# Performance work log

Hardware: AMD Instinct MI355X
Metric: run time of the kernel (lower is better)

Reference implementation:

```python
import jax, jax.numpy as jnp
import numpy as np

N = 50000      # nodes
E = 500000     # edges
H = 128        # hidden_channels
P = 1024       # number of (src,dst) link pairs: z==1 and z==2 counts
L = 3          # num_layers
MAXZ = 1000


def setup_inputs() -> dict:
    key = jax.random.key(0)
    ks = jax.random.split(key, 16)
    # z: P src nodes (label 1), P dst nodes (label 2), rest random labels >= 3
    z = jnp.concatenate([
        jnp.ones((P,), jnp.int32),
        jnp.full((P,), 2, jnp.int32),
        jax.random.randint(ks[0], (N - 2 * P,), 3, MAXZ, dtype=jnp.int32),
    ])
    edge_index = jax.random.randint(ks[1], (2, E), 0, N, dtype=jnp.int32)
    batch = jnp.zeros((N,), jnp.int32)  # unused in executed branch
    s = 1.0 / np.sqrt(H)
    z_table = jax.random.normal(ks[2], (MAXZ, H), jnp.float32) * 0.1
    conv_Wl = jax.random.normal(ks[3], (L, H, H), jnp.float32) * s
    conv_bl = jax.random.normal(ks[4], (L, H), jnp.float32) * 0.01
    conv_Wr = jax.random.normal(ks[5], (L, H, H), jnp.float32) * s
    W0 = jax.random.normal(ks[6], (H, H), jnp.float32) * s
    b0 = jax.random.normal(ks[7], (H,), jnp.float32) * 0.01
    W1 = jax.random.normal(ks[8], (H, H), jnp.float32) * s
    b1 = jax.random.normal(ks[9], (H,), jnp.float32) * 0.01
    W2 = jax.random.normal(ks[10], (1, H), jnp.float32) * s
    b2 = jax.random.normal(ks[11], (1,), jnp.float32) * 0.01
    return dict(z=z, edge_index=edge_index, batch=batch, z_table=z_table,
                conv_Wl=conv_Wl, conv_bl=conv_bl, conv_Wr=conv_Wr,
                W0=W0, b0=b0, W1=W1, b1=b1, W2=W2, b2=b2)


def _sage_conv(x, Wl, bl, Wr, src, dst):
    # x: [2, N, H]; mean-aggregate neighbor messages then linear (PyG SAGEConv)
    msgs = x[:, src, :]  # [2, E, H] gather
    agg = jax.vmap(lambda m: jax.ops.segment_sum(m, dst, num_segments=N))(msgs)
    deg = jax.ops.segment_sum(jnp.ones((dst.shape[0],), x.dtype), dst, num_segments=N)
    agg = agg / jnp.maximum(deg, 1.0)[None, :, None]
    return agg @ Wl.T + bl + x @ Wr.T  # lin_l(mean) + bias + lin_r(x)


def reference(z, edge_index, batch, z_table, conv_Wl, conv_bl, conv_Wr,
              W0, b0, W1, b1, W2, b2):
    src, dst = edge_index[0], edge_index[1]
    # ([[1],[2]] == z).long() -> [2, N] in {0,1}; embed -> [2, N, H]
    lbl = (jnp.arange(1, 3, dtype=z.dtype)[:, None] == z[None, :]).astype(jnp.int32)
    x = z_table[lbl]
    for i in range(L - 1):
        x = jax.nn.relu(_sage_conv(x, conv_Wl[i], conv_bl[i], conv_Wr[i], src, dst))
    x = _sage_conv(x, conv_Wl[L - 1], conv_bl[L - 1], conv_Wr[L - 1], src, dst)
    h = jax.nn.relu(x @ W0.T + b0).sum(axis=0)  # [N, H]
    src_idx = jnp.nonzero(z == 1, size=P)[0]
    dst_idx = jnp.nonzero(z == 2, size=P)[0]
    p = h[src_idx] * h[dst_idx]                 # [P, H]
    return jax.nn.relu(p @ W1.T + b1) @ W2.T + b2  # [P, 1]
```

## Files before the change

### kernel.cpp

```cpp
#include <hip/hip_runtime.h>
#include <stdint.h>

#define HH 128
typedef unsigned long long ull;
typedef unsigned short u16;

__device__ __forceinline__ ull shfl_up64(ull v, int d) {
  unsigned lo = (unsigned)__shfl_up((int)(unsigned)(v & 0xffffffffULL), d);
  unsigned hi = (unsigned)__shfl_up((int)(unsigned)(v >> 32), d);
  return ((ull)hi << 32) | (ull)lo;
}
__device__ __forceinline__ ull shfl_down64(ull v, int d) {
  unsigned lo = (unsigned)__shfl_down((int)(unsigned)(v & 0xffffffffULL), d);
  unsigned hi = (unsigned)__shfl_down((int)(unsigned)(v >> 32), d);
  return ((ull)hi << 32) | (ull)lo;
}

__global__ __launch_bounds__(256) void k_ytab(
    const float* __restrict__ zt, const float* __restrict__ Wl0,
    const float* __restrict__ Wr0, const float* __restrict__ Wl2,
    const float* __restrict__ Wr2, const float* __restrict__ bl0,
    const float* __restrict__ bl1, float* __restrict__ y_l,
    float* __restrict__ y_rb, float* __restrict__ vecs_g,
    const int* __restrict__ z, int N, ull* __restrict__ cnt64,
    int* __restrict__ mark) {
  __shared__ float ztS[2][HH];
  __shared__ float vS[4][HH];
  __shared__ float xS[16][HH];
  int t = threadIdx.x;
  {
    int gid = blockIdx.x * 256 + t;
    int nthr = gridDim.x * 256;
    for (int n = gid; n < N; n += nthr) {
      cnt64[n] = 0ULL;
      mark[n] = (z[n] <= 2) ? 1 : 0;
    }
  }
  ztS[t >> 7][t & 127] = zt[t];
  __syncthreads();
#pragma unroll
  for (int rep = 0; rep < 2; rep++) {
    int idx = t + rep * 256;
    int m = idx >> 7, j = idx & 127;
    const float* W = (m < 2) ? Wl0 : Wr0;
    const float* zrow = ztS[m & 1];
    float acc = 0.f;
    for (int k = 0; k < HH; k++) acc = fmaf(zrow[k], W[j * HH + k], acc);
    vS[m][j] = acc;
  }
  __syncthreads();
  if (blockIdx.x == 0) {
    vecs_g[t] = vS[t >> 7][t & 127];
    vecs_g[256 + t] = vS[2 + (t >> 7)][t & 127];
  }
  int v0 = blockIdx.x * 16;
#pragma unroll
  for (int rep = 0; rep < 8; rep++) {
    int idx = t + rep * 256;
    int r = idx >> 7, j = idx & 127;
    int v = v0 + r;
    int d = v >> 4, cnt = (v >> 1) & 7, sel = v & 1;
    float invd = 1.0f / (float)max(d, 1);
    float u1 = (float)cnt * invd, u0 = (float)(d - cnt) * invd;
    xS[r][j] = fmaxf(fmaf(u0, vS[0][j], fmaf(u1, vS[1][j], bl0[j] + vS[2 + sel][j])), 0.f);
  }
  __syncthreads();
  int j = t & 127, rh = t >> 7;
  float al[8], ar[8];
#pragma unroll
  for (int q = 0; q < 8; q++) { al[q] = 0.f; ar[q] = 0.f; }
  for (int k = 0; k < HH; k++) {
    float wl = Wl2[j * HH + k], wr = Wr2[j * HH + k];
#pragma unroll
    for (int q = 0; q < 8; q++) {
      float x = xS[rh * 8 + q][k];
      al[q] = fmaf(x, wl, al[q]);
      ar[q] = fmaf(x, wr, ar[q]);
    }
  }
  float bb = bl1[j];
#pragma unroll
  for (int q = 0; q < 8; q++) {
    int v = v0 + rh * 8 + q;
    y_l[((size_t)v << 7) + j] = al[q];
    y_rb[((size_t)v << 7) + j] = ar[q] + bb;
  }
}

__global__ void k_edge(const int* __restrict__ z, const int* __restrict__ src,
                       const int* __restrict__ dst, int E,
                       ull* __restrict__ cnt64, int* __restrict__ mark,
                       int* __restrict__ pos) {
  int tid = blockIdx.x * blockDim.x + threadIdx.x;
  int stride = gridDim.x * blockDim.x;
  for (int e = tid; e < E; e += stride) {
    int s = src[e], d = dst[e];
    int zs = z[s];
    ull val = 1ULL | ((ull)(zs == 1) << 20) | ((ull)(zs == 2) << 40);
    ull old = atomicAdd(&cnt64[d], val);
    pos[e] = (int)(old & 0xFFFFF);
    if (z[d] <= 2) mark[s] = 1;
  }
}

__global__ void k_scan1(const ull* __restrict__ cnt64, const int* __restrict__ mark,
                        const int* __restrict__ z, int N,
                        ull* __restrict__ locout, ull* __restrict__ partials) {
  __shared__ ull wsum[4];
  int t = threadIdx.x, b = blockIdx.x;
  int base = b * 1024 + t * 4;
  ull l[4]; ull s = 0;
  for (int i = 0; i < 4; i++) {
    int idx = base + i; ull v = 0;
    if (idx < N) {
      int zz = z[idx];
      v = (cnt64[idx] & 0xFFFFFULL) | ((ull)mark[idx] << 20)
        | ((ull)(zz == 1) << 40) | ((ull)(zz == 2) << 52);
    }
    l[i] = s; s += v;
  }
  int lane = t & 63, wid = t >> 6;
  ull vi = s;
  for (int d2 = 1; d2 < 64; d2 <<= 1) { ull o = shfl_up64(vi, d2); if (lane >= d2) vi += o; }
  if (lane == 63) wsum[wid] = vi;
  __syncthreads();
  ull woff = 0;
  for (int w = 0; w < wid; w++) woff += wsum[w];
  ull thrbase = woff + vi - s;
  for (int i = 0; i < 4; i++) {
    int idx = base + i;
    if (idx < N) locout[idx] = thrbase + l[i];
  }
  if (t == 255) partials[b] = woff + vi;
}

__global__ __launch_bounds__(256) void k_post(const ull* __restrict__ locout, const ull* __restrict__ partials,
                       const int* __restrict__ z, const int* __restrict__ mark,
                       const ull* __restrict__ cnt64,
                       int N, int P, int* __restrict__ rowptr, int* __restrict__ mlist,
                       int* __restrict__ minv, int* __restrict__ plist,
                       int* __restrict__ Rm, int4* __restrict__ pack,
                       u16* __restrict__ keyN) {
  __shared__ ull base_s;
  int t = threadIdx.x;
  if (t < 64) {
    int need = blockIdx.x >> 2;
    ull v = (t < need) ? partials[t] : 0ULL;
    for (int o = 32; o > 0; o >>= 1) v += shfl_down64(v, o);
    if (t == 0) base_s = v;
  }
  __syncthreads();
  int n = blockIdx.x * 256 + t;
  if (n >= N) return;
  ull s = locout[n] + base_s;
  int rp = (int)(s & 0xFFFFF);
  int mp = (int)((s >> 20) & 0xFFFFF);
  int r1 = (int)((s >> 40) & 0xFFF);
  int r2 = (int)(s >> 52);
  rowptr[n] = rp;
  int mk = mark[n];
  if (mk) { mlist[mp] = n; minv[n] = mp; }
  int zz = z[n];
  if (zz == 1) plist[r1] = n;
  else if (zz == 2) plist[P + r2] = n;
  ull cv = cnt64[n];
  int dd = (int)(cv & 0xFFFFF), c1 = (int)((cv >> 20) & 0xFFFFF), c2 = (int)((cv >> 40) & 0xFFFFF);
  pack[n] = make_int4(dd, c1, c2, zz);
  int wcls = (zz == 1) ? 1 : ((zz == 2) ? 2 : 0);
  u16 key;
  if (dd < 64 && c1 < 8 && c2 < 8) key = (u16)(dd | (c1 << 6) | (c2 << 9) | (wcls << 12));
  else key = 0x8000;
  keyN[n] = key;
  if (n == N - 1) *Rm = mp + mk;
}

__global__ void k_csrk(const int* __restrict__ src, const int* __restrict__ dst, int E,
                       const int* __restrict__ rowptr, const int* __restrict__ pos,
                       const u16* __restrict__ keyN, ull* __restrict__ csrk) {
  int e = blockIdx.x * blockDim.x + threadIdx.x;
  if (e >= E) return;
  int d = dst[e], s = src[e];
  csrk[rowptr[d] + pos[e]] = (ull)(unsigned)s | ((ull)keyN[s] << 32);
}

__device__ __noinline__ float4 yrow_fb(const float* __restrict__ vecs,
    const float* __restrict__ bl0, const float* __restrict__ Wm,
    int j4, int d, int cnt, int sel) {
  float invd = 1.0f / (float)max(d, 1);
  float u1 = (float)cnt * invd, u0 = (float)(d - cnt) * invd;
  const float* Rv = vecs + (2 + sel) * HH;
  float4 acc = make_float4(0, 0, 0, 0);
  for (int k = 0; k < HH; k++) {
    float x = fmaxf(fmaf(u0, vecs[k], fmaf(u1, vecs[HH + k], bl0[k] + Rv[k])), 0.f);
    acc.x = fmaf(x, Wm[(j4 + 0) * HH + k], acc.x);
    acc.y = fmaf(x, Wm[(j4 + 1) * HH + k], acc.y);
    acc.z = fmaf(x, Wm[(j4 + 2) * HH + k], acc.z);
    acc.w = fmaf(x, Wm[(j4 + 3) * HH + k], acc.w);
  }
  return acc;
}

__device__ __forceinline__ float4 yl_fetch(ull cv, int ch, int chsel, int j4,
    const float* __restrict__ y_l, const int4* __restrict__ pack,
    const float* __restrict__ vecs, const float* __restrict__ bl0,
    const float* __restrict__ Wl2) {
  int key = (int)(cv >> 32);
  if (key & 0x8000) {
    int s = (int)(cv & 0xFFFFFFFFULL);
    int4 p = pack[s];
    int cc = ch ? p.z : p.y;
    int sel = (p.w == chsel) ? 1 : 0;
    return yrow_fb(vecs, bl0, Wl2, j4, p.x, cc, sel);
  }
  int cc = (key >> (6 + 3 * ch)) & 7;
  int sel = (((key >> 12) & 3) == chsel) ? 1 : 0;
  int row = ((key & 63) << 4) + (cc << 1) + sel;
  return *(const float4*)(y_l + ((size_t)row << 7) + j4);
}

__global__ __launch_bounds__(256) void k_agg2Y(const int4* __restrict__ pack,
    const ull* __restrict__ csrk, const float* __restrict__ y_l,
    const float* __restrict__ y_rb, const float* __restrict__ vecs,
    const float* __restrict__ bl0, const float* __restrict__ bl1,
    const float* __restrict__ Wl2, const float* __restrict__ Wr2,
    const int* __restrict__ rowptr, const int* __restrict__ mlist,
    const int* __restrict__ Rdev, float* __restrict__ x2c) {
  int gt = blockIdx.x * blockDim.x + threadIdx.x;
  int w = gt >> 6, lane = gt & 63;
  int nw = (gridDim.x * blockDim.x) >> 6;
  int T = *Rdev;
  int ch = lane >> 5, j4 = (lane & 31) * 4;
  int chsel = ch + 1;
  for (int task = w; task < T; task += nw) {
    int n = mlist[task];
    int4 pn = pack[n];
    int beg = rowptr[n], d = pn.x;
    float4 acc = make_float4(0, 0, 0, 0);
    int i = 0;
    for (; i + 4 <= d; i += 4) {
      ull c0 = csrk[beg + i], c1 = csrk[beg + i + 1];
      ull c2 = csrk[beg + i + 2], c3 = csrk[beg + i + 3];
      float4 v0 = yl_fetch(c0, ch, chsel, j4, y_l, pack, vecs, bl0, Wl2);
      float4 v1 = yl_fetch(c1, ch, chsel, j4, y_l, pack, vecs, bl0, Wl2);
      float4 v2 = yl_fetch(c2, ch, chsel, j4, y_l, pack, vecs, bl0, Wl2);
      float4 v3 = yl_fetch(c3, ch, chsel, j4, y_l, pack, vecs, bl0, Wl2);
      acc.x += v0.x + v1.x + v2.x + v3.x;
      acc.y += v0.y + v1.y + v2.y + v3.y;
      acc.z += v0.z + v1.z + v2.z + v3.z;
      acc.w += v0.w + v1.w + v2.w + v3.w;
    }
    for (; i < d; i++) {
      float4 v0 = yl_fetch(csrk[beg + i], ch, chsel, j4, y_l, pack, vecs, bl0, Wl2);
      acc.x += v0.x; acc.y += v0.y; acc.z += v0.z; acc.w += v0.w;
    }
    float inv = 1.0f / (float)max(d, 1);
    int ccn = ch ? pn.z : pn.y;
    int seln = (pn.w == chsel) ? 1 : 0;
    float4 yr;
    if (pn.x < 64 && ccn < 8) {
      yr = *(const float4*)(y_rb + ((size_t)(((pn.x << 3) + ccn) * 2 + seln) << 7) + j4);
    } else {
      yr = yrow_fb(vecs, bl0, Wr2, j4, pn.x, ccn, seln);
      yr.x += bl1[j4]; yr.y += bl1[j4 + 1]; yr.z += bl1[j4 + 2]; yr.w += bl1[j4 + 3];
    }
    float4 o;
    o.x = fmaxf(fmaf(acc.x, inv, yr.x), 0.f);
    o.y = fmaxf(fmaf(acc.y, inv, yr.y), 0.f);
    o.z = fmaxf(fmaf(acc.z, inv, yr.z), 0.f);
    o.w = fmaxf(fmaf(acc.w, inv, yr.w), 0.f);
    *(float4*)(x2c + (size_t)task * 256 + ch * HH + j4) = o;
  }
}

__global__ __launch_bounds__(256) void k_agg3(const float* __restrict__ x2c,
    const ull* __restrict__ csrk, const int* __restrict__ rowptr,
    const int4* __restrict__ pack, const int* __restrict__ plist,
    const int* __restrict__ minv, int T, float* __restrict__ aggp) {
  int gt = blockIdx.x * blockDim.x + threadIdx.x;
  int w = gt >> 6, lane = gt & 63;
  int nw = (gridDim.x * blockDim.x) >> 6;
  int j4 = lane * 4;
  for (int task = w; task < T; task += nw) {
    int n = plist[task];
    int beg = rowptr[n], d = pack[n].x;
    float4 acc = make_float4(0, 0, 0, 0);
    int i = 0;
    for (; i + 4 <= d; i += 4) {
      int m0 = minv[(int)(csrk[beg + i] & 0xFFFFFFFFULL)];
      int m1 = minv[(int)(csrk[beg + i + 1] & 0xFFFFFFFFULL)];
      int m2 = minv[(int)(csrk[beg + i + 2] & 0xFFFFFFFFULL)];
      int m3 = minv[(int)(csrk[beg + i + 3] & 0xFFFFFFFFULL)];
      float4 v0 = *(const float4*)(x2c + (size_t)m0 * 256 + j4);
      float4 v1 = *(const float4*)(x2c + (size_t)m1 * 256 + j4);
      float4 v2 = *(const float4*)(x2c + (size_t)m2 * 256 + j4);
      float4 v3 = *(const float4*)(x2c + (size_t)m3 * 256 + j4);
      acc.x += v0.x + v1.x + v2.x + v3.x;
      acc.y += v0.y + v1.y + v2.y + v3.y;
      acc.z += v0.z + v1.z + v2.z + v3.z;
      acc.w += v0.w + v1.w + v2.w + v3.w;
    }
    for (; i < d; i++) {
      int m0 = minv[(int)(csrk[beg + i] & 0xFFFFFFFFULL)];
      float4 v0 = *(const float4*)(x2c + (size_t)m0 * 256 + j4);
      acc.x += v0.x; acc.y += v0.y; acc.z += v0.z; acc.w += v0.w;
    }
    float inv = 1.0f / (float)max(d, 1);
    float4 o = make_float4(acc.x * inv, acc.y * inv, acc.z * inv, acc.w * inv);
    *(float4*)(aggp + (size_t)task * 256 + j4) = o;
  }
}

#define G3 4
__global__ __launch_bounds__(256) void k_gemm3F(const float* __restrict__ aggp,
    const float* __restrict__ x2c, const float* __restrict__ Wl3,
    const float* __restrict__ Wr3, const float* __restrict__ W0,
    const float* __restrict__ bl2, const float* __restrict__ b0,
    const int* __restrict__ plist, const int* __restrict__ minv,
    float* __restrict__ tmp0) {
  __shared__ float aS[G3][256], xS[G3][256], x3S[G3][256];
  __shared__ float wAS[32][HH + 1], wBS[32][HH + 1];
  int t = threadIdx.x;
  int i0 = blockIdx.x * G3;
  int j = t & 127, c = t >> 7;
#pragma unroll
  for (int g = 0; g < G3; g++) {
    int i = i0 + g;
    aS[g][t] = aggp[(size_t)i * 256 + t];
    xS[g][t] = x2c[(size_t)minv[plist[i]] * 256 + t];
  }
  float acc[G3];
#pragma unroll
  for (int g = 0; g < G3; g++) acc[g] = bl2[j];
  int jw = t >> 3;
  int kk0 = (t & 7) * 4;
  for (int kt = 0; kt < 4; kt++) {
    __syncthreads();
#pragma unroll
    for (int q = 0; q < 4; q++) {
      int jj = q * 32 + jw;
      float4 va = *(const float4*)(Wl3 + (size_t)jj * HH + kt * 32 + kk0);
      float4 vb = *(const float4*)(Wr3 + (size_t)jj * HH + kt * 32 + kk0);
      wAS[kk0 + 0][jj] = va.x; wAS[kk0 + 1][jj] = va.y;
      wAS[kk0 + 2][jj] = va.z; wAS[kk0 + 3][jj] = va.w;
      wBS[kk0 + 0][jj] = vb.x; wBS[kk0 + 1][jj] = vb.y;
      wBS[kk0 + 2][jj] = vb.z; wBS[kk0 + 3][jj] = vb.w;
    }
    __syncthreads();
#pragma unroll
    for (int kk = 0; kk < 32; kk++) {
      int k = kt * 32 + kk;
      float wl = wAS[kk][j], wr = wBS[kk][j];
#pragma unroll
      for (int g = 0; g < G3; g++)
        acc[g] = fmaf(aS[g][c * HH + k], wl, fmaf(xS[g][c * HH + k], wr, acc[g]));
    }
  }
#pragma unroll
  for (int g = 0; g < G3; g++) x3S[g][t] = acc[g];
  float acc2[G3];
#pragma unroll
  for (int g = 0; g < G3; g++) acc2[g] = b0[j];
  for (int kt = 0; kt < 4; kt++) {
    __syncthreads();
#pragma unroll
    for (int q = 0; q < 4; q++) {
      int jj = q * 32 + jw;
      float4 v0 = *(const float4*)(W0 + (size_t)jj * HH + kt * 32 + kk0);
      wAS[kk0 + 0][jj] = v0.x; wAS[kk0 + 1][jj] = v0.y;
      wAS[kk0 + 2][jj] = v0.z; wAS[kk0 + 3][jj] = v0.w;
    }
    __syncthreads();
#pragma unroll
    for (int kk = 0; kk < 32; kk++) {
      int k = kt * 32 + kk;
      float w0v = wAS[kk][j];
#pragma unroll
      for (int g = 0; g < G3; g++)
        acc2[g] = fmaf(x3S[g][c * HH + k], w0v, acc2[g]);
    }
  }
#pragma unroll
  for (int g = 0; g < G3; g++)
    tmp0[(size_t)(2 * (i0 + g) + c) * HH + j] = fmaxf(acc2[g], 0.f);
}

__global__ __launch_bounds__(256) void k_finalP(const float* __restrict__ tmp0,
    const float* __restrict__ W1, const float* __restrict__ b1,
    const float* __restrict__ W2, const float* __restrict__ b2,
    int P, float* __restrict__ out) {
  __shared__ float pS[2][HH];
  __shared__ float wred[4];
  int t = threadIdx.x;
  int half = t >> 7, j = t & 127;
  int i = blockIdx.x * 2 + half;
  float hs = tmp0[(size_t)(2 * i) * HH + j] + tmp0[(size_t)(2 * i + 1) * HH + j];
  float hd = tmp0[(size_t)(2 * (i + P)) * HH + j] + tmp0[(size_t)(2 * (i + P) + 1) * HH + j];
  pS[half][j] = hs * hd;
  __syncthreads();
  float acc = b1[j];
#pragma unroll 8
  for (int k = 0; k < HH; k++) acc = fmaf(pS[half][k], W1[j * HH + k], acc);
  float v = fmaxf(acc, 0.f) * W2[j];
  for (int off = 32; off > 0; off >>= 1) v += __shfl_down(v, off);
  int wid = t >> 6, lane = t & 63;
  if (lane == 0) wred[wid] = v;
  __syncthreads();
  if (t == 0) out[i] = wred[0] + wred[1] + b2[0];
  else if (t == 128) out[i] = wred[2] + wred[3] + b2[0];
}

extern "C" void kernel_launch(void* const* d_in, const int* in_sizes, int n_in,
                              void* d_out, int out_size, void* d_ws, size_t ws_size,
                              hipStream_t stream) {
  const int* z = (const int*)d_in[0];
  const int* ei = (const int*)d_in[1];
  const float* z_table = (const float*)d_in[3];
  const float* conv_Wl = (const float*)d_in[4];
  const float* conv_bl = (const float*)d_in[5];
  const float* conv_Wr = (const float*)d_in[6];
  const float* W0 = (const float*)d_in[7];
  const float* b0 = (const float*)d_in[8];
  const float* W1 = (const float*)d_in[9];
  const float* b1 = (const float*)d_in[10];
  const float* W2 = (const float*)d_in[11];
  const float* b2 = (const float*)d_in[12];
  float* out = (float*)d_out;

  int N = in_sizes[0];
  int E = in_sizes[1] / 2;
  int P = out_size;
  int P2 = 2 * P;
  const int* srcA = ei;
  const int* dstA = ei + E;

  char* basep = (char*)d_ws;
  size_t off = 0;
  auto alloc = [&](size_t bytes) -> char* {
    off = (off + 255) & ~(size_t)255;
    char* pp = basep + off; off += bytes; return pp;
  };
  float* y_l   = (float*)alloc((size_t)1024 * HH * 4);
  float* y_rb  = (float*)alloc((size_t)1024 * HH * 4);
  float* vecs  = (float*)alloc((size_t)4 * HH * 4);
  float* x2c   = (float*)alloc((size_t)N * 256 * 4);
  float* aggp  = (float*)alloc((size_t)P2 * 256 * 4);
  float* tmp0  = (float*)alloc((size_t)2 * P2 * HH * 4);
  ull*   cnt64 = (ull*)alloc((size_t)N * 8);
  int*   mark  = (int*)alloc((size_t)N * 4);
  int*   pos   = (int*)alloc((size_t)E * 4);
  int*   rowptr= (int*)alloc((size_t)N * 4);
  int*   mlist = (int*)alloc((size_t)N * 4);
  int*   minv  = (int*)alloc((size_t)N * 4);
  int*   plist = (int*)alloc((size_t)P2 * 4);
  ull*   csrk  = (ull*)alloc((size_t)E * 8);
  ull*   locout= (ull*)alloc((size_t)N * 8);
  ull*   partials = (ull*)alloc(256 * 8);
  int*   Rm_dev = (int*)alloc(256);
  u16*   keyN  = (u16*)alloc((size_t)N * 2);
  int4*  pack  = (int4*)alloc((size_t)N * 16);
  (void)ws_size; (void)n_in;

  k_ytab<<<64, 256, 0, stream>>>(z_table, conv_Wl, conv_Wr,
                                 conv_Wl + HH * HH, conv_Wr + HH * HH,
                                 conv_bl, conv_bl + HH, y_l, y_rb, vecs,
                                 z, N, cnt64, mark);
  k_edge<<<1024, 256, 0, stream>>>(z, srcA, dstA, E, cnt64, mark, pos);
  int nb = (N + 1023) / 1024;
  k_scan1<<<nb, 256, 0, stream>>>(cnt64, mark, z, N, locout, partials);
  k_post<<<(N + 255) / 256, 256, 0, stream>>>(locout, partials, z, mark, cnt64, N, P,
                                              rowptr, mlist, minv, plist, Rm_dev, pack, keyN);
  k_csrk<<<(E + 255) / 256, 256, 0, stream>>>(srcA, dstA, E, rowptr, pos, keyN, csrk);
  k_agg2Y<<<2048, 256, 0, stream>>>(pack, csrk, y_l, y_rb, vecs, conv_bl, conv_bl + HH,
                                    conv_Wl + HH * HH, conv_Wr + HH * HH,
                                    rowptr, mlist, Rm_dev, x2c);
  k_agg3<<<512, 256, 0, stream>>>(x2c, csrk, rowptr, pack, plist, minv, P2, aggp);
  k_gemm3F<<<P2 / G3, 256, 0, stream>>>(aggp, x2c, conv_Wl + 2 * HH * HH,
                                        conv_Wr + 2 * HH * HH, W0,
                                        conv_bl + 2 * HH, b0, plist, minv, tmp0);
  k_finalP<<<P / 2, 256, 0, stream>>>(tmp0, W1, b1, W2, b2, P, out);
}
```

Baseline: 132.7 us.

## Stage weight tiles in LDS with coalesced loads; skip CSR writes for unmarked dsts

```diff
diff --git a/kernel.cpp b/kernel.cpp
--- a/kernel.cpp
+++ b/kernel.cpp
@@ -27,6 +27,7 @@
   __shared__ float ztS[2][HH];
   __shared__ float vS[4][HH];
   __shared__ float xS[16][HH];
+  __shared__ float wAS[32][HH + 1], wBS[32][HH + 1];
   int t = threadIdx.x;
   {
     int gid = blockIdx.x * 256 + t;
@@ -38,16 +39,32 @@
   }
   ztS[t >> 7][t & 127] = zt[t];
   __syncthreads();
-#pragma unroll
-  for (int rep = 0; rep < 2; rep++) {
-    int idx = t + rep * 256;
-    int m = idx >> 7, j = idx & 127;
-    const float* W = (m < 2) ? Wl0 : Wr0;
-    const float* zrow = ztS[m & 1];
-    float acc = 0.f;
-    for (int k = 0; k < HH; k++) acc = fmaf(zrow[k], W[j * HH + k], acc);
-    vS[m][j] = acc;
-  }
+  int j = t & 127, half = t >> 7;
+  int jw = t >> 3, kk0 = (t & 7) * 4;
+  float accA = 0.f, accR = 0.f;
+  for (int kt = 0; kt < 4; kt++) {
+    __syncthreads();
+#pragma unroll
+    for (int q = 0; q < 4; q++) {
+      int jj = q * 32 + jw;
+      float4 va = *(const float4*)(Wl0 + (size_t)jj * HH + kt * 32 + kk0);
+      float4 vb = *(const float4*)(Wr0 + (size_t)jj * HH + kt * 32 + kk0);
+      wAS[kk0 + 0][jj] = va.x; wAS[kk0 + 1][jj] = va.y;
+      wAS[kk0 + 2][jj] = va.z; wAS[kk0 + 3][jj] = va.w;
+      wBS[kk0 + 0][jj] = vb.x; wBS[kk0 + 1][jj] = vb.y;
+      wBS[kk0 + 2][jj] = vb.z; wBS[kk0 + 3][jj] = vb.w;
+    }
+    __syncthreads();
+#pragma unroll
+    for (int kk = 0; kk < 32; kk++) {
+      float zk = ztS[half][kt * 32 + kk];
+      accA = fmaf(zk, wAS[kk][j], accA);
+      accR = fmaf(zk, wBS[kk][j], accR);
+    }
+  }
+  __syncthreads();
+  vS[half][j] = accA;
+  vS[2 + half][j] = accR;
   __syncthreads();
   if (blockIdx.x == 0) {
     vecs_g[t] = vS[t >> 7][t & 127];
@@ -57,25 +74,39 @@
 #pragma unroll
   for (int rep = 0; rep < 8; rep++) {
     int idx = t + rep * 256;
-    int r = idx >> 7, j = idx & 127;
+    int r = idx >> 7, jx = idx & 127;
     int v = v0 + r;
     int d = v >> 4, cnt = (v >> 1) & 7, sel = v & 1;
     float invd = 1.0f / (float)max(d, 1);
     float u1 = (float)cnt * invd, u0 = (float)(d - cnt) * invd;
-    xS[r][j] = fmaxf(fmaf(u0, vS[0][j], fmaf(u1, vS[1][j], bl0[j] + vS[2 + sel][j])), 0.f);
-  }
-  __syncthreads();
-  int j = t & 127, rh = t >> 7;
+    xS[r][jx] = fmaxf(fmaf(u0, vS[0][jx], fmaf(u1, vS[1][jx], bl0[jx] + vS[2 + sel][jx])), 0.f);
+  }
+  int rh = t >> 7;
   float al[8], ar[8];
 #pragma unroll
   for (int q = 0; q < 8; q++) { al[q] = 0.f; ar[q] = 0.f; }
-  for (int k = 0; k < HH; k++) {
-    float wl = Wl2[j * HH + k], wr = Wr2[j * HH + k];
-#pragma unroll
-    for (int q = 0; q < 8; q++) {
-      float x = xS[rh * 8 + q][k];
-      al[q] = fmaf(x, wl, al[q]);
-      ar[q] = fmaf(x, wr, ar[q]);
+  for (int kt = 0; kt < 4; kt++) {
+    __syncthreads();
+#pragma unroll
+    for (int q = 0; q < 4; q++) {
+      int jj = q * 32 + jw;
+      float4 va = *(const float4*)(Wl2 + (size_t)jj * HH + kt * 32 + kk0);
+      float4 vb = *(const float4*)(Wr2 + (size_t)jj * HH + kt * 32 + kk0);
+      wAS[kk0 + 0][jj] = va.x; wAS[kk0 + 1][jj] = va.y;
+      wAS[kk0 + 2][jj] = va.z; wAS[kk0 + 3][jj] = va.w;
+      wBS[kk0 + 0][jj] = vb.x; wBS[kk0 + 1][jj] = vb.y;
+      wBS[kk0 + 2][jj] = vb.z; wBS[kk0 + 3][jj] = vb.w;
+    }
+    __syncthreads();
+#pragma unroll
+    for (int kk = 0; kk < 32; kk++) {
+      float wl = wAS[kk][j], wr = wBS[kk][j];
+#pragma unroll
+      for (int q = 0; q < 8; q++) {
+        float x = xS[rh * 8 + q][kt * 32 + kk];
+        al[q] = fmaf(x, wl, al[q]);
+        ar[q] = fmaf(x, wr, ar[q]);
+      }
     }
   }
   float bb = bl1[j];
@@ -176,10 +207,13 @@
 
 __global__ void k_csrk(const int* __restrict__ src, const int* __restrict__ dst, int E,
                        const int* __restrict__ rowptr, const int* __restrict__ pos,
-                       const u16* __restrict__ keyN, ull* __restrict__ csrk) {
+                       const u16* __restrict__ keyN, const int* __restrict__ mark,
+                       ull* __restrict__ csrk) {
   int e = blockIdx.x * blockDim.x + threadIdx.x;
   if (e >= E) return;
-  int d = dst[e], s = src[e];
+  int d = dst[e];
+  if (!mark[d]) return;
+  int s = src[e];
   csrk[rowptr[d] + pos[e]] = (ull)(unsigned)s | ((ull)keyN[s] << 32);
 }
 
@@ -389,6 +423,7 @@
     const float* __restrict__ W2, const float* __restrict__ b2,
     int P, float* __restrict__ out) {
   __shared__ float pS[2][HH];
+  __shared__ float wAS[32][HH + 1];
   __shared__ float wred[4];
   int t = threadIdx.x;
   int half = t >> 7, j = t & 127;
@@ -396,10 +431,22 @@
   float hs = tmp0[(size_t)(2 * i) * HH + j] + tmp0[(size_t)(2 * i + 1) * HH + j];
   float hd = tmp0[(size_t)(2 * (i + P)) * HH + j] + tmp0[(size_t)(2 * (i + P) + 1) * HH + j];
   pS[half][j] = hs * hd;
-  __syncthreads();
+  int jw = t >> 3, kk0 = (t & 7) * 4;
   float acc = b1[j];
-#pragma unroll 8
-  for (int k = 0; k < HH; k++) acc = fmaf(pS[half][k], W1[j * HH + k], acc);
+  for (int kt = 0; kt < 4; kt++) {
+    __syncthreads();
+#pragma unroll
+    for (int q = 0; q < 4; q++) {
+      int jj = q * 32 + jw;
+      float4 v = *(const float4*)(W1 + (size_t)jj * HH + kt * 32 + kk0);
+      wAS[kk0 + 0][jj] = v.x; wAS[kk0 + 1][jj] = v.y;
+      wAS[kk0 + 2][jj] = v.z; wAS[kk0 + 3][jj] = v.w;
+    }
+    __syncthreads();
+#pragma unroll
+    for (int kk = 0; kk < 32; kk++)
+      acc = fmaf(pS[half][kt * 32 + kk], wAS[kk][j], acc);
+  }
   float v = fmaxf(acc, 0.f) * W2[j];
   for (int off = 32; off > 0; off >>= 1) v += __shfl_down(v, off);
   int wid = t >> 6, lane = t & 63;
@@ -469,7 +516,7 @@
   k_scan1<<<nb, 256, 0, stream>>>(cnt64, mark, z, N, locout, partials);
   k_post<<<(N + 255) / 256, 256, 0, stream>>>(locout, partials, z, mark, cnt64, N, P,
                                               rowptr, mlist, minv, plist, Rm_dev, pack, keyN);
-  k_csrk<<<(E + 255) / 256, 256, 0, stream>>>(srcA, dstA, E, rowptr, pos, keyN, csrk);
+  k_csrk<<<(E + 255) / 256, 256, 0, stream>>>(srcA, dstA, E, rowptr, pos, keyN, mark, csrk);
   k_agg2Y<<<2048, 256, 0, stream>>>(pack, csrk, y_l, y_rb, vecs, conv_bl, conv_bl + HH,
                                     conv_Wl + HH * HH, conv_Wr + HH * HH,
                                     rowptr, mlist, Rm_dev, x2c);
```

Result: faster. 128.1 us (-3.5%).
